# Kernel tuning notes

Hardware: AMD Instinct MI355X
Metric: run time of the kernel (lower is better)

Reference implementation:

```python
import jax, jax.numpy as jnp
import numpy as np

N = 50000       # nodes
E = 400000      # edges (avg degree 8)
IN, HID, OUT, ED = 128, 256, 128, 64
EXP = 2          # GENConv MLP expansion
EPS_MSG = 1e-7   # GENConv eps added to relu(msg)
EPS_BN = 1e-5    # BatchNorm eps
EPS_SM = 1e-16   # PyG softmax denominator eps


def _lin(key, fi, fo):
    w = jax.random.normal(key, (fi, fo), jnp.float32) / np.float32(np.sqrt(fi))
    return w, jnp.zeros((fo,), jnp.float32)


def _layer_params(key, fi, fo, ed):
    ks = jax.random.split(key, 5)
    Wsrc, bsrc = _lin(ks[0], fi, fo)
    Wdst, bdst = _lin(ks[1], fi, fo)
    We, be = _lin(ks[2], ed, fo)
    W1, b1 = _lin(ks[3], fo, fo * EXP)
    W2, b2 = _lin(ks[4], fo * EXP, fo)
    g = jnp.ones((fo * EXP,), jnp.float32)   # BN gamma
    bt = jnp.zeros((fo * EXP,), jnp.float32) # BN beta
    return dict(Wsrc=Wsrc, bsrc=bsrc, Wdst=Wdst, bdst=bdst, We=We, be=be,
                W1=W1, b1=b1, g=g, bt=bt, W2=W2, b2=b2)


def setup_inputs() -> dict:
    key = jax.random.key(0)
    k0, k1, k2, k3, k4 = jax.random.split(key, 5)
    inp = {
        'x': jax.random.normal(k0, (N, IN), jnp.float32),
        'edge_index': jax.random.randint(k1, (2, E), 0, N, jnp.int32),
        'edge_attr': jax.random.normal(k2, (E, ED), jnp.float32),
    }
    for pref, p in (('l1_', _layer_params(k3, IN, HID, ED)),
                    ('l2_', _layer_params(k4, HID, OUT, ED))):
        for n, v in p.items():
            inp[pref + n] = v
    return inp


def _genconv(x, src, dst, ea, Wsrc, bsrc, Wdst, bdst, We, be, W1, b1, g, bt, W2, b2):
    n = x.shape[0]
    h = x @ Wsrc + bsrc                          # [N, F] lin_src
    e = ea @ We + be                             # [E, F] lin_edge
    msg = jax.nn.relu(h[src] + e) + EPS_MSG      # [E, F] message
    # softmax aggregation over destination nodes (t = 1.0)
    mx = jax.ops.segment_max(msg, dst, num_segments=n)
    ex = jnp.exp(msg - mx[dst])
    den = jax.ops.segment_sum(ex, dst, num_segments=n)
    alpha = ex / (den[dst] + EPS_SM)
    agg = jax.ops.segment_sum(alpha * msg, dst, num_segments=n)  # [N, F]
    out = agg + (x @ Wdst + bdst)                # residual lin_dst
    # MLP: Linear -> BatchNorm(train stats) -> ReLU -> Linear
    h1 = out @ W1 + b1                           # [N, 2F]
    mu = h1.mean(0)
    var = h1.var(0)
    h1 = (h1 - mu) * jax.lax.rsqrt(var + EPS_BN) * g + bt
    return jax.nn.relu(h1) @ W2 + b2


def reference(x, edge_index, edge_attr,
              l1_Wsrc, l1_bsrc, l1_Wdst, l1_bdst, l1_We, l1_be,
              l1_W1, l1_b1, l1_g, l1_bt, l1_W2, l1_b2,
              l2_Wsrc, l2_bsrc, l2_Wdst, l2_bdst, l2_We, l2_be,
              l2_W1, l2_b1, l2_g, l2_bt, l2_W2, l2_b2):
    src, dst = edge_index[0], edge_index[1]
    h = _genconv(x, src, dst, edge_attr,
                 l1_Wsrc, l1_bsrc, l1_Wdst, l1_bdst, l1_We, l1_be,
                 l1_W1, l1_b1, l1_g, l1_bt, l1_W2, l1_b2)
    h = jax.nn.relu(h)
    return _genconv(h, src, dst, edge_attr,
                    l2_Wsrc, l2_bsrc, l2_Wdst, l2_bdst, l2_We, l2_be,
                    l2_W1, l2_b1, l2_g, l2_bt, l2_W2, l2_b2)
```

## Files before the change

kernel.cpp:

```cpp
#include <hip/hip_runtime.h>

typedef unsigned short u16;
typedef unsigned int u32;
typedef __attribute__((ext_vector_type(8))) short sv8;
typedef __attribute__((ext_vector_type(4))) float fv4;
typedef __attribute__((ext_vector_type(4))) unsigned short us4;
typedef __attribute__((ext_vector_type(2))) unsigned short us2;

__device__ __forceinline__ u16 f2b(float x) {
    union { float f; u32 u; } a; a.f = x;
    u32 r = a.u + 0x7FFFu + ((a.u >> 16) & 1u);
    return (u16)(r >> 16);
}
__device__ __forceinline__ float b2f(u16 h) {
    union { u32 u; float f; } a; a.u = ((u32)h) << 16;
    return a.f;
}

__device__ __forceinline__ void gll16(const void* g, void* l) {
    __builtin_amdgcn_global_load_lds((__attribute__((address_space(1))) void*)g,
                                     (__attribute__((address_space(3))) void*)l,
                                     16, 0, 0);
}

template<bool AF32, bool AAFF, int EPI, bool STATS>
__global__ __launch_bounds__(256) void k_gemm(
    const void* __restrict__ Aptr, const u16* __restrict__ Wt,
    const float* __restrict__ bias, void* __restrict__ Cptr,
    int M, int K, int F,
    const float* __restrict__ sc, const float* __restrict__ sh,
    float* __restrict__ sums, float* __restrict__ sumsq)
{
    __shared__ u16 As[64][68];
    __shared__ u16 Bs[64][68];
    __shared__ u16 Cs[64][68];
    const int t = threadIdx.x, w = t >> 6, l = t & 63;

    const int gx = gridDim.x;
    const int nwg = gx * gridDim.y;
    const int bid = blockIdx.y * gx + blockIdx.x;
    const int qq = nwg >> 3, rr = nwg & 7;
    const int xcd = bid & 7, jj = bid >> 3;
    const int swz = (xcd < rr ? xcd * (qq + 1) : rr * (qq + 1) + (xcd - rr) * qq) + jj;
    const int n0 = (swz % gx) * 64;
    const int m0 = (swz / gx) * 64;

    const int arow = t >> 2;
    const size_t gr = (size_t)(m0 + arow < M ? m0 + arow : M - 1);

    fv4 acc[4] = {};

    for (int k0 = 0; k0 < K; k0 += 64) {
        #pragma unroll
        for (int i = 0; i < 2; ++i) {
            const int acol = (((t & 3) << 1) + i) << 3;
            const int kb = k0 + acol;
            sv8 av;
            if constexpr (AF32) {
                const float* Af = (const float*)Aptr;
                fv4 u0 = *(const fv4*)(Af + gr * K + kb);
                fv4 u1 = *(const fv4*)(Af + gr * K + kb + 4);
                #pragma unroll
                for (int j = 0; j < 4; ++j) { av[j] = (short)f2b(u0[j]); av[j + 4] = (short)f2b(u1[j]); }
            } else if constexpr (AAFF) {
                sv8 v = *(const sv8*)((const u16*)Aptr + gr * K + kb);
                fv4 c0 = *(const fv4*)(sc + kb), c1 = *(const fv4*)(sc + kb + 4);
                fv4 d0 = *(const fv4*)(sh + kb), d1 = *(const fv4*)(sh + kb + 4);
                #pragma unroll
                for (int j = 0; j < 4; ++j) {
                    av[j]     = (short)f2b(fmaxf(b2f((u16)v[j])     * c0[j] + d0[j], 0.f));
                    av[j + 4] = (short)f2b(fmaxf(b2f((u16)v[j + 4]) * c1[j] + d1[j], 0.f));
                }
            } else {
                av = *(const sv8*)((const u16*)Aptr + gr * K + kb);
            }
            *(sv8*)&As[arow][acol] = av;
            *(sv8*)&Bs[arow][acol] = *(const sv8*)(Wt + (size_t)(n0 + arow) * K + kb);
        }
        __syncthreads();

        #pragma unroll
        for (int kk = 0; kk < 2; ++kk) {
            sv8 a = *(const sv8*)&As[(w << 4) + (l & 15)][((kk << 2) + (l >> 4)) << 3];
            #pragma unroll
            for (int ct = 0; ct < 4; ++ct) {
                sv8 b = *(const sv8*)&Bs[(ct << 4) + (l & 15)][((kk << 2) + (l >> 4)) << 3];
                acc[ct] = __builtin_amdgcn_mfma_f32_16x16x32_bf16(a, b, acc[ct], 0, 0, 0);
            }
        }
        __syncthreads();
    }

    const int lr0 = (w << 4) + ((l >> 4) << 2);
    #pragma unroll
    for (int ct = 0; ct < 4; ++ct) {
        const int col = (ct << 4) + (l & 15);
        const float bv = bias[n0 + col];
        float s = 0.f, s2 = 0.f;
        #pragma unroll
        for (int r = 0; r < 4; ++r) {
            const int lrow = lr0 + r;
            const bool valid = (m0 + lrow) < M;
            float v = acc[ct][r] + bv;
            if constexpr (STATS) { if (valid) { s += v; s2 += v * v; } }
            if constexpr (EPI == 1) v = fmaxf(v, 0.f);
            if constexpr (EPI == 3) {
                if (valid) ((float*)Cptr)[(size_t)(m0 + lrow) * F + n0 + col] = v;
            } else {
                Cs[lrow][col] = f2b(v);
            }
        }
        if constexpr (STATS) {
            s  += __shfl_xor(s, 16);  s  += __shfl_xor(s, 32);
            s2 += __shfl_xor(s2, 16); s2 += __shfl_xor(s2, 32);
            if (l < 16) { unsafeAtomicAdd(&sums[n0 + col], s); unsafeAtomicAdd(&sumsq[n0 + col], s2); }
        }
    }
    if constexpr (EPI != 3) {
        __syncthreads();
        const int lrow = t >> 2, c0 = (t & 3) << 4;
        if (m0 + lrow < M) {
            u16* Cb = (u16*)Cptr + (size_t)(m0 + lrow) * F + n0 + c0;
            *(sv8*)Cb       = *(const sv8*)&Cs[lrow][c0];
            *(sv8*)(Cb + 8) = *(const sv8*)&Cs[lrow][c0 + 8];
        }
    }
}

template<int FN>
__global__ __launch_bounds__(256) void k_egemm3(
    const float* __restrict__ ea, const int* __restrict__ perm,
    const u16* __restrict__ Wt, const float* __restrict__ bias,
    u16* __restrict__ Cbuf)
{
    __shared__ u16 Bs[FN * 64];
    const int t = threadIdx.x, w = t >> 6, l = t & 63;
    const int m0 = blockIdx.x * 64;

    constexpr int BISS = FN / 32;
    #pragma unroll
    for (int i = 0; i < BISS; ++i) {
        int slot = ((w * BISS + i) << 6) + l;
        int row = slot >> 3, g = (slot & 7) ^ (row & 7);
        gll16(Wt + (size_t)row * 64 + g * 8, Bs + ((w * BISS + i) << 6) * 8);
    }

    const int g0 = l >> 4;
    const int gr = m0 + (w << 4) + (l & 15);
    const int prow = perm[gr];
    const float* ar = ea + (size_t)prow * 64 + (g0 << 3);
    fv4 u0 = *(const fv4*)ar;
    fv4 u1 = *(const fv4*)(ar + 4);
    fv4 u2 = *(const fv4*)(ar + 32);
    fv4 u3 = *(const fv4*)(ar + 36);
    sv8 a0, a1;
    #pragma unroll
    for (int j = 0; j < 4; ++j) {
        a0[j] = (short)f2b(u0[j]); a0[j + 4] = (short)f2b(u1[j]);
        a1[j] = (short)f2b(u2[j]); a1[j + 4] = (short)f2b(u3[j]);
    }
    __syncthreads();

    fv4 acc[FN / 16];
    #pragma unroll
    for (int ct = 0; ct < FN / 16; ++ct) {
        int Brow = (ct << 4) + (l & 15);
        sv8 b0 = *(const sv8*)&Bs[(Brow * 8 + ((g0)     ^ (Brow & 7))) * 8];
        sv8 b1 = *(const sv8*)&Bs[(Brow * 8 + ((g0 + 4) ^ (Brow & 7))) * 8];
        fv4 z = {};
        z = __builtin_amdgcn_mfma_f32_16x16x32_bf16(a0, b0, z, 0, 0, 0);
        acc[ct] = __builtin_amdgcn_mfma_f32_16x16x32_bf16(a1, b1, z, 0, 0, 0);
    }

    const int r0 = (w << 4) + ((l >> 4) << 2);
    #pragma unroll
    for (int ct = 0; ct < FN / 16; ++ct) {
        const int col = (ct << 4) + (l & 15);
        const float bv = bias[col];
        #pragma unroll
        for (int r = 0; r < 4; ++r) {
            const int row = m0 + r0 + r;
            u32 my = (u32)f2b(acc[ct][r] + bv);
            u32 ot = (u32)__shfl_xor((int)my, 1);
            if (!(l & 1))
                *(u32*)(Cbuf + (size_t)row * FN + col) = (my & 0xFFFFu) | (ot << 16);
        }
    }
}

__global__ void k_hist(const int* __restrict__ dst, int* __restrict__ counts, int E) {
    int i = blockIdx.x * 256 + threadIdx.x;
    if (i < E) atomicAdd(&counts[dst[i]], 1);
}

__global__ __launch_bounds__(256) void k_psum(const int* __restrict__ counts,
                                              int* __restrict__ bsum, int n) {
    int i = blockIdx.x * 256 + threadIdx.x;
    int v = (i < n) ? counts[i] : 0;
    #pragma unroll
    for (int o = 1; o < 64; o <<= 1) v += __shfl_xor(v, o);
    __shared__ int ws[4];
    if ((threadIdx.x & 63) == 0) ws[threadIdx.x >> 6] = v;
    __syncthreads();
    if (threadIdx.x == 0) bsum[blockIdx.x] = ws[0] + ws[1] + ws[2] + ws[3];
}

__global__ __launch_bounds__(256) void k_bscan(const int* __restrict__ bsum,
                                               int* __restrict__ boff, int nb) {
    __shared__ int sm[256];
    int t = threadIdx.x;
    int v = (t < nb) ? bsum[t] : 0;
    sm[t] = v; __syncthreads();
    #pragma unroll
    for (int o = 1; o < 256; o <<= 1) {
        int u = (t >= o) ? sm[t - o] : 0;
        __syncthreads();
        sm[t] += u;
        __syncthreads();
    }
    if (t < nb) boff[t] = sm[t] - v;
}

__global__ __launch_bounds__(256) void k_windp(const int* __restrict__ counts,
                                               const int* __restrict__ boff,
                                               int* __restrict__ indptr,
                                               int* __restrict__ cursors, int n) {
    __shared__ int sm[256];
    const int t = threadIdx.x, i = blockIdx.x * 256 + t;
    int v = (i < n) ? counts[i] : 0;
    sm[t] = v; __syncthreads();
    #pragma unroll
    for (int o = 1; o < 256; o <<= 1) {
        int u = (t >= o) ? sm[t - o] : 0;
        __syncthreads();
        sm[t] += u;
        __syncthreads();
    }
    int excl = sm[t] - v + boff[blockIdx.x];
    if (i < n) { indptr[i] = excl; cursors[i] = excl; }
    if (i == n - 1) indptr[n] = excl + v;
}

__global__ void k_scatter(const int* __restrict__ dst, const int* __restrict__ src,
                          int* __restrict__ cursors, int* __restrict__ perm,
                          int* __restrict__ srcp, int E) {
    int i = blockIdx.x * 256 + threadIdx.x;
    if (i < E) {
        int p = atomicAdd(&cursors[dst[i]], 1);
        perm[p] = i;
        srcp[p] = src[i];
    }
}

template<int F, int VPT>
__global__ __launch_bounds__(256) void k_agg(
    const u16* __restrict__ e, const u16* __restrict__ hhd,
    const int* __restrict__ srcp, const int* __restrict__ indptr,
    u16* __restrict__ out, int N)
{
    const int nid = blockIdx.x * 4 + (threadIdx.x >> 6);
    if (nid >= N) return;
    const int c0 = (threadIdx.x & 63) * VPT;
    const int S = 2 * F;
    const int p0 = indptr[nid], p1 = indptr[nid + 1];
    float den[VPT] = {}, num[VPT] = {};

    auto LOADP = [&](int p, u16* ev, u16* hv) {
        const int s = srcp[p];
        if constexpr (VPT == 4) {
            *(us4*)ev = *(const us4*)&e[(size_t)p * F + c0];
            *(us4*)hv = *(const us4*)&hhd[(size_t)s * S + c0];
        } else {
            *(us2*)ev = *(const us2*)&e[(size_t)p * F + c0];
            *(us2*)hv = *(const us2*)&hhd[(size_t)s * S + c0];
        }
    };
    auto ACCUM = [&](const u16* ev, const u16* hv) {
        #pragma unroll
        for (int j = 0; j < VPT; ++j) {
            float x = fmaxf(b2f(ev[j]) + b2f(hv[j]), 0.f) + 1e-7f;
            float ex = __expf(x);
            den[j] += ex;
            num[j] += ex * x;
        }
    };

    if (p0 < p1) {
        u16 ev[VPT], hv[VPT];
        LOADP(p0, ev, hv);
        for (int p = p0 + 1; p < p1; ++p) {
            u16 ev2[VPT], hv2[VPT];
            LOADP(p, ev2, hv2);
            ACCUM(ev, hv);
            #pragma unroll
            for (int j = 0; j < VPT; ++j) { ev[j] = ev2[j]; hv[j] = hv2[j]; }
        }
        ACCUM(ev, hv);
    }

    #pragma unroll
    for (int j = 0; j < VPT; ++j) {
        float o = num[j] / (den[j] + 1e-16f) + b2f(hhd[(size_t)nid * S + F + c0 + j]);
        out[(size_t)nid * F + c0 + j] = f2b(o);
    }
}

struct WtDesc { const float* W; u16* D; int K; int F; int end; };
struct WtPack { WtDesc d[10]; };

__global__ void k_wtall(WtPack p, int total) {
    int i = blockIdx.x * 256 + threadIdx.x;
    if (i >= total) return;
    int s = 0, base = 0;
    while (i >= p.d[s].end) { base = p.d[s].end; ++s; }
    int loc = i - base;
    int K = p.d[s].K, F = p.d[s].F;
    int f = loc / K, k = loc - f * K;
    p.d[s].D[loc] = f2b(p.d[s].W[(size_t)k * F + f]);
}

__global__ void k_bcat(const float* __restrict__ bsrc1, const float* __restrict__ bdst1,
                       const float* __restrict__ bsrc2, const float* __restrict__ bdst2,
                       float* __restrict__ bcat1, float* __restrict__ bcat2) {
    int t = threadIdx.x;
    bcat1[t] = bsrc1[t];
    bcat1[256 + t] = bdst1[t];
    if (t < 128) {
        bcat2[t] = bsrc2[t];
        bcat2[128 + t] = bdst2[t];
    }
}

__global__ void k_bnfinal(const float* __restrict__ sums, const float* __restrict__ sumsq,
                          const float* __restrict__ g, const float* __restrict__ bt,
                          float* __restrict__ scale, float* __restrict__ shift,
                          int C, float invN)
{
    int c = blockIdx.x * 256 + threadIdx.x;
    if (c < C) {
        float mu  = sums[c] * invN;
        float var = sumsq[c] * invN - mu * mu;
        float s   = g[c] * rsqrtf(var + 1e-5f);
        scale[c] = s;
        shift[c] = bt[c] - mu * s;
    }
}

extern "C" void kernel_launch(void* const* d_in, const int* in_sizes, int n_in,
                              void* d_out, int out_size, void* d_ws, size_t ws_size,
                              hipStream_t stream)
{
    const int IN = 128, HID = 256, OUT = 128, ED = 64;
    const int N = in_sizes[0] / IN;
    const int E = in_sizes[1] / 2;

    const float* x   = (const float*)d_in[0];
    const int*   src = (const int*)d_in[1];
    const int*   dst = src + E;
    const float* ea  = (const float*)d_in[2];
    auto F32 = [&](int i) { return (const float*)d_in[i]; };
    const float *Wsrc1 = F32(3),  *bsrc1 = F32(4),  *Wdst1 = F32(5),  *bdst1 = F32(6),
                *We1   = F32(7),  *be1   = F32(8),  *W11   = F32(9),  *b11   = F32(10),
                *g1    = F32(11), *bt1   = F32(12), *W21   = F32(13), *b21   = F32(14);
    const float *Wsrc2 = F32(15), *bsrc2 = F32(16), *Wdst2 = F32(17), *bdst2 = F32(18),
                *We2   = F32(19), *be2   = F32(20), *W12   = F32(21), *b12   = F32(22),
                *g2    = F32(23), *bt2   = F32(24), *W22   = F32(25), *b22   = F32(26);

    char* wp = (char*)d_ws;
    auto carve = [&](size_t bytes) -> void* {
        void* r = (void*)wp; wp += (bytes + 255) & ~(size_t)255; return r;
    };
    u16* wcat1  = (u16*)carve((size_t)HID * IN * 2);
    u16* wdst1t = (u16*)carve((size_t)HID * IN * 2);
    u16* we1t   = (u16*)carve((size_t)HID * ED * 2);
    u16* w11t   = (u16*)carve((size_t)(2 * HID) * HID * 2);
    u16* w21t   = (u16*)carve((size_t)HID * (2 * HID) * 2);
    u16* wcat2  = (u16*)carve((size_t)OUT * HID * 2);
    u16* wdst2t = (u16*)carve((size_t)OUT * HID * 2);
    u16* we2t   = (u16*)carve((size_t)OUT * ED * 2);
    u16* w12t   = (u16*)carve((size_t)(2 * OUT) * OUT * 2);
    u16* w22t   = (u16*)carve((size_t)OUT * (2 * OUT) * 2);
    int* counts  = (int*)carve((size_t)N * 4);
    int* indptr  = (int*)carve((size_t)(N + 1) * 4);
    int* cursors = (int*)carve((size_t)N * 4);
    int* perm    = (int*)carve((size_t)E * 4);
    int* srcp    = (int*)carve((size_t)E * 4);
    int* bsum    = (int*)carve((size_t)256 * 4);
    int* boff    = (int*)carve((size_t)256 * 4);
    u16* hhd  = (u16*)carve((size_t)N * 512 * 2);
    u16* x2   = (u16*)carve((size_t)N * HID * 2);
    u16* ebuf = (u16*)carve((size_t)E * HID * 2);
    float* stats1 = (float*)carve((size_t)1024 * 4);
    float* stats2 = (float*)carve((size_t)512 * 4);
    float* ss1    = (float*)carve((size_t)1024 * 4);
    float* ss2    = (float*)carve((size_t)512 * 4);
    float* bcat1  = (float*)carve((size_t)512 * 4);
    float* bcat2  = (float*)carve((size_t)256 * 4);
    u16* h1 = ebuf;

    hipMemsetAsync(counts, 0, (size_t)N * 4, stream);
    hipMemsetAsync(stats1, 0, (size_t)(1024 + 512) * 4, stream);
    k_hist<<<dim3((E + 255) / 256), dim3(256), 0, stream>>>(dst, counts, E);
    const int nb = (N + 255) / 256;
    k_psum<<<dim3(nb), dim3(256), 0, stream>>>(counts, bsum, N);
    k_bscan<<<dim3(1), dim3(256), 0, stream>>>(bsum, boff, nb);
    k_windp<<<dim3(nb), dim3(256), 0, stream>>>(counts, boff, indptr, cursors, N);
    k_scatter<<<dim3((E + 255) / 256), dim3(256), 0, stream>>>(dst, src, cursors, perm, srcp, E);

    WtPack wpk; int acc_end = 0;
    auto addw = [&](int idx, const float* W, u16* D, int K, int F) {
        acc_end += K * F;
        wpk.d[idx] = WtDesc{W, D, K, F, acc_end};
    };
    addw(0, Wsrc1, wcat1,  IN, HID);   addw(1, Wdst1, wdst1t, IN, HID);
    addw(2, We1,   we1t,   ED, HID);   addw(3, W11,   w11t,   HID, 2 * HID);
    addw(4, W21,   w21t,   2 * HID, HID);
    addw(5, Wsrc2, wcat2,  HID, OUT);  addw(6, Wdst2, wdst2t, HID, OUT);
    addw(7, We2,   we2t,   ED, OUT);   addw(8, W12,   w12t,   OUT, 2 * OUT);
    addw(9, W22,   w22t,   2 * OUT, OUT);
    k_wtall<<<dim3((acc_end + 255) / 256), dim3(256), 0, stream>>>(wpk, acc_end);
    k_bcat<<<dim3(1), dim3(256), 0, stream>>>(bsrc1, bdst1, bsrc2, bdst2, bcat1, bcat2);

    const int gm = (N + 63) / 64;

    k_gemm<true, false, 0, false><<<dim3(8, gm), dim3(256), 0, stream>>>(
        x, wcat1, bcat1, hhd, N, IN, 512, nullptr, nullptr, nullptr, nullptr);
    k_egemm3<256><<<dim3(E / 64), dim3(256), 0, stream>>>(ea, perm, we1t, be1, ebuf);
    k_agg<256, 4><<<dim3((N + 3) / 4), dim3(256), 0, stream>>>(ebuf, hhd, srcp, indptr, x2, N);
    k_gemm<false, false, 0, true><<<dim3(8, gm), dim3(256), 0, stream>>>(
        x2, w11t, b11, h1, N, HID, 512, nullptr, nullptr, stats1, stats1 + 512);
    k_bnfinal<<<dim3(2), dim3(256), 0, stream>>>(
        stats1, stats1 + 512, g1, bt1, ss1, ss1 + 512, 512, 1.f / N);
    k_gemm<false, true, 1, false><<<dim3(4, gm), dim3(256), 0, stream>>>(
        h1, w21t, b21, x2, N, 512, HID, ss1, ss1 + 512, nullptr, nullptr);

    k_gemm<false, false, 0, false><<<dim3(4, gm), dim3(256), 0, stream>>>(
        x2, wcat2, bcat2, hhd, N, HID, 256, nullptr, nullptr, nullptr, nullptr);
    k_egemm3<128><<<dim3(E / 64), dim3(256), 0, stream>>>(ea, perm, we2t, be2, ebuf);
    k_agg<128, 2><<<dim3((N + 3) / 4), dim3(256), 0, stream>>>(ebuf, hhd, srcp, indptr, x2, N);
    k_gemm<false, false, 0, true><<<dim3(4, gm), dim3(256), 0, stream>>>(
        x2, w12t, b12, h1, N, OUT, 256, nullptr, nullptr, stats2, stats2 + 256);
    k_bnfinal<<<dim3(1), dim3(256), 0, stream>>>(
        stats2, stats2 + 256, g2, bt2, ss2, ss2 + 256, 256, 1.f / N);
    k_gemm<false, true, 3, false><<<dim3(2, gm), dim3(256), 0, stream>>>(
        h1, w22t, b22, d_out, N, HID, OUT, ss2, ss2 + 256, nullptr, nullptr);
}
```

Baseline: 677.1 us.

## Use direct global-to-LDS loads with XOR swizzle in GEMM; prefetch src indices in aggregation

The GEMM now loads weight tiles, and plain bf16 A tiles, straight into LDS with global_load_lds, skipping the register round trip. Both tiles use an XOR-swizzled unpadded layout to avoid bank conflicts without padding. The aggregation kernel reads the next edge's source index one iteration early, so the dependent gather of hhd is not held up by the index load. The swizzle has to be applied consistently on store and read, and the f32 and affine A paths still go through registers.

```diff
diff --git a/kernel.cpp b/kernel.cpp
--- a/kernel.cpp
+++ b/kernel.cpp
@@ -31,8 +31,8 @@
     const float* __restrict__ sc, const float* __restrict__ sh,
     float* __restrict__ sums, float* __restrict__ sumsq)
 {
-    __shared__ u16 As[64][68];
-    __shared__ u16 Bs[64][68];
+    __shared__ u16 As[64 * 64];
+    __shared__ u16 Bs[64 * 64];
     __shared__ u16 Cs[64][68];
     const int t = threadIdx.x, w = t >> 6, l = t & 63;
 
@@ -45,46 +45,68 @@
     const int n0 = (swz % gx) * 64;
     const int m0 = (swz / gx) * 64;
 
-    const int arow = t >> 2;
-    const size_t gr = (size_t)(m0 + arow < M ? m0 + arow : M - 1);
-
     fv4 acc[4] = {};
 
     for (int k0 = 0; k0 < K; k0 += 64) {
         #pragma unroll
         for (int i = 0; i < 2; ++i) {
-            const int acol = (((t & 3) << 1) + i) << 3;
-            const int kb = k0 + acol;
-            sv8 av;
-            if constexpr (AF32) {
-                const float* Af = (const float*)Aptr;
-                fv4 u0 = *(const fv4*)(Af + gr * K + kb);
-                fv4 u1 = *(const fv4*)(Af + gr * K + kb + 4);
-                #pragma unroll
-                for (int j = 0; j < 4; ++j) { av[j] = (short)f2b(u0[j]); av[j + 4] = (short)f2b(u1[j]); }
-            } else if constexpr (AAFF) {
-                sv8 v = *(const sv8*)((const u16*)Aptr + gr * K + kb);
-                fv4 c0 = *(const fv4*)(sc + kb), c1 = *(const fv4*)(sc + kb + 4);
-                fv4 d0 = *(const fv4*)(sh + kb), d1 = *(const fv4*)(sh + kb + 4);
-                #pragma unroll
-                for (int j = 0; j < 4; ++j) {
-                    av[j]     = (short)f2b(fmaxf(b2f((u16)v[j])     * c0[j] + d0[j], 0.f));
-                    av[j + 4] = (short)f2b(fmaxf(b2f((u16)v[j + 4]) * c1[j] + d1[j], 0.f));
+            const int sb = (w * 2 + i) << 6;
+            const int slot = sb + l;
+            const int row = slot >> 3;
+            const int gs = (slot & 7) ^ (row & 7);
+            gll16(Wt + (size_t)(n0 + row) * K + k0 + gs * 8, Bs + sb * 8);
+        }
+        if constexpr (!AF32 && !AAFF) {
+            const u16* Ab = (const u16*)Aptr;
+            #pragma unroll
+            for (int i = 0; i < 2; ++i) {
+                const int sb = (w * 2 + i) << 6;
+                const int slot = sb + l;
+                const int row = slot >> 3;
+                const int gs = (slot & 7) ^ (row & 7);
+                int rg = m0 + row; if (rg > M - 1) rg = M - 1;
+                gll16(Ab + (size_t)rg * K + k0 + gs * 8, As + sb * 8);
+            }
+        } else {
+            const int row = t >> 2;
+            int rg = m0 + row; if (rg > M - 1) rg = M - 1;
+            const size_t gr = (size_t)rg;
+            #pragma unroll
+            for (int i = 0; i < 2; ++i) {
+                const int g = ((t & 3) << 1) + i;
+                const int kb = k0 + (g << 3);
+                sv8 av;
+                if constexpr (AF32) {
+                    const float* Af = (const float*)Aptr;
+                    fv4 u0 = *(const fv4*)(Af + gr * K + kb);
+                    fv4 u1 = *(const fv4*)(Af + gr * K + kb + 4);
+                    #pragma unroll
+                    for (int j = 0; j < 4; ++j) { av[j] = (short)f2b(u0[j]); av[j + 4] = (short)f2b(u1[j]); }
+                } else {
+                    sv8 v = *(const sv8*)((const u16*)Aptr + gr * K + kb);
+                    fv4 c0 = *(const fv4*)(sc + kb), c1 = *(const fv4*)(sc + kb + 4);
+                    fv4 d0 = *(const fv4*)(sh + kb), d1 = *(const fv4*)(sh + kb + 4);
+                    #pragma unroll
+                    for (int j = 0; j < 4; ++j) {
+                        av[j]     = (short)f2b(fmaxf(b2f((u16)v[j])     * c0[j] + d0[j], 0.f));
+                        av[j + 4] = (short)f2b(fmaxf(b2f((u16)v[j + 4]) * c1[j] + d1[j], 0.f));
+                    }
                 }
-            } else {
-                av = *(const sv8*)((const u16*)Aptr + gr * K + kb);
+                const int gs = g ^ (row & 7);
+                *(sv8*)&As[(row * 8 + gs) * 8] = av;
             }
-            *(sv8*)&As[arow][acol] = av;
-            *(sv8*)&Bs[arow][acol] = *(const sv8*)(Wt + (size_t)(n0 + arow) * K + kb);
         }
         __syncthreads();
 
         #pragma unroll
         for (int kk = 0; kk < 2; ++kk) {
-            sv8 a = *(const sv8*)&As[(w << 4) + (l & 15)][((kk << 2) + (l >> 4)) << 3];
+            const int Arow = (w << 4) + (l & 15);
+            const int ga = (kk << 2) + (l >> 4);
+            sv8 a = *(const sv8*)&As[(Arow * 8 + (ga ^ (Arow & 7))) * 8];
             #pragma unroll
             for (int ct = 0; ct < 4; ++ct) {
-                sv8 b = *(const sv8*)&Bs[(ct << 4) + (l & 15)][((kk << 2) + (l >> 4)) << 3];
+                const int Brow = (ct << 4) + (l & 15);
+                sv8 b = *(const sv8*)&Bs[(Brow * 8 + (ga ^ (Brow & 7))) * 8];
                 acc[ct] = __builtin_amdgcn_mfma_f32_16x16x32_bf16(a, b, acc[ct], 0, 0, 0);
             }
         }
@@ -265,15 +287,13 @@
     const int p0 = indptr[nid], p1 = indptr[nid + 1];
     float den[VPT] = {}, num[VPT] = {};
 
-    auto LOADP = [&](int p, u16* ev, u16* hv) {
-        const int s = srcp[p];
-        if constexpr (VPT == 4) {
-            *(us4*)ev = *(const us4*)&e[(size_t)p * F + c0];
-            *(us4*)hv = *(const us4*)&hhd[(size_t)s * S + c0];
-        } else {
-            *(us2*)ev = *(const us2*)&e[(size_t)p * F + c0];
-            *(us2*)hv = *(const us2*)&hhd[(size_t)s * S + c0];
-        }
+    auto LOADE = [&](int p, u16* ev) {
+        if constexpr (VPT == 4) *(us4*)ev = *(const us4*)&e[(size_t)p * F + c0];
+        else                    *(us2*)ev = *(const us2*)&e[(size_t)p * F + c0];
+    };
+    auto LOADH = [&](int s, u16* hv) {
+        if constexpr (VPT == 4) *(us4*)hv = *(const us4*)&hhd[(size_t)s * S + c0];
+        else                    *(us2*)hv = *(const us2*)&hhd[(size_t)s * S + c0];
     };
     auto ACCUM = [&](const u16* ev, const u16* hv) {
         #pragma unroll
@@ -286,16 +306,19 @@
     };
 
     if (p0 < p1) {
-        u16 ev[VPT], hv[VPT];
-        LOADP(p0, ev, hv);
+        int sB = (p0 + 1 < p1) ? srcp[p0 + 1] : 0;
+        u16 evA[VPT], hvA[VPT];
+        LOADE(p0, evA); LOADH(srcp[p0], hvA);
         for (int p = p0 + 1; p < p1; ++p) {
-            u16 ev2[VPT], hv2[VPT];
-            LOADP(p, ev2, hv2);
-            ACCUM(ev, hv);
+            int sC = (p + 1 < p1) ? srcp[p + 1] : 0;
+            u16 evB[VPT], hvB[VPT];
+            LOADE(p, evB); LOADH(sB, hvB);
+            ACCUM(evA, hvA);
             #pragma unroll
-            for (int j = 0; j < VPT; ++j) { ev[j] = ev2[j]; hv[j] = hv2[j]; }
-        }
-        ACCUM(ev, hv);
+            for (int j = 0; j < VPT; ++j) { evA[j] = evB[j]; hvA[j] = hvB[j]; }
+            sB = sC;
+        }
+        ACCUM(evA, hvA);
     }
 
     #pragma unroll
```

After: 669.5 us. No clear change (-1.1%).
